# Performance work log

Hardware: AMD Instinct MI355X
Metric: run time of the kernel (lower is better)

## Reference

```python
import jax, jax.numpy as jnp
import numpy as np

B, V = 128, 128000

def setup_inputs() -> dict:
    key = jax.random.key(0)
    k1, k2, k3, k4 = jax.random.split(key, 4)
    logits = jax.random.normal(k1, (B, V), dtype=jnp.float32) * 4.0
    k = jax.random.randint(k2, (B,), 1, 64).astype(jnp.int32)
    p = jax.random.uniform(k3, (B,), dtype=jnp.float32, minval=0.5, maxval=1.0)
    # torch's q.exponential_(): Exp(1) noise = -log(U)
    u = jax.random.uniform(k4, (B, V), dtype=jnp.float32, minval=1e-10, maxval=1.0)
    exp_noise = -jnp.log(u)
    return {"logits": logits, "k": k, "p": p, "exp_noise": exp_noise}

def _apply_top_k_top_p(logits, k, p):
    # ascending sort, matching torch logits.sort(descending=False)
    idx = jnp.argsort(logits, axis=-1)                       # [B, V]
    logits_sort = jnp.take_along_axis(logits, idx, axis=-1)  # [B, V]
    # top-k: threshold is the (V-k)-th smallest value; everything below -> -inf
    thr_pos = (logits.shape[-1] - k.astype(jnp.int32))[:, None]       # [B, 1]
    thr = jnp.take_along_axis(logits_sort, thr_pos, axis=-1)          # [B, 1]
    logits_sort = jnp.where(logits_sort < thr, -jnp.inf, logits_sort)
    # top-p: drop the low-probability tail whose cumulative mass <= 1 - p
    probs_sort = jax.nn.softmax(logits_sort, axis=-1)
    probs_sum = jnp.cumsum(probs_sort, axis=-1)
    top_p_mask = probs_sum <= (1.0 - p)[:, None]
    top_p_mask = top_p_mask.at[:, -1].set(False)  # always keep the max token
    logits_sort = jnp.where(top_p_mask, -jnp.inf, logits_sort)
    # scatter filtered values back to original token positions
    inv = jnp.argsort(idx, axis=-1)
    return jnp.take_along_axis(logits_sort, inv, axis=-1)

def reference(logits, k, p, exp_noise):
    filtered = _apply_top_k_top_p(logits, k, p)
    probs = jax.nn.softmax(filtered.astype(jnp.float32), axis=-1)
    # random_sample: argmax(probs / Exp(1)) == Gumbel-trick categorical sample
    return jnp.argmax(probs / exp_noise, axis=-1)
```

## Files before the change

kernel.cpp:

```cpp
#include <hip/hip_runtime.h>
#include <stdint.h>

#define B_ROWS 128
#define V_COLS 128000
#define BPR 16
#define SLICE (V_COLS / BPR)
#define N4 (SLICE / 4)
#define K1_THREADS 256
#define CAP 2048

__device__ __forceinline__ uint32_t f2u_bits(uint32_t x) {
    return (x & 0x80000000u) ? ~x : (x | 0x80000000u);
}
__device__ __forceinline__ float u2f(uint32_t u) {
    uint32_t x = (u & 0x80000000u) ? (u & 0x7FFFFFFFu) : ~u;
    return __uint_as_float(x);
}

__device__ __forceinline__ bool pair_gt(uint32_t au, uint32_t ai, uint32_t bu, uint32_t bi) {
    return (au > bu) || (au == bu && ai > bi);
}

__device__ __forceinline__ void bitonic_sort_desc(uint32_t* su, uint32_t* si, int NP) {
    const int tid = threadIdx.x;
    const int nth = blockDim.x;
    for (int ksz = 2; ksz <= NP; ksz <<= 1) {
        for (int j = ksz >> 1; j > 0; j >>= 1) {
            __syncthreads();
            for (int i = tid; i < NP; i += nth) {
                int ixj = i ^ j;
                if (ixj > i) {
                    uint32_t ua = su[i], ub = su[ixj];
                    uint32_t ia = si[i], ib = si[ixj];
                    bool a_lt = (ua < ub) || (ua == ub && ia < ib);
                    if (((i & ksz) == 0) ? a_lt : !a_lt) {
                        su[i] = ub; su[ixj] = ua;
                        si[i] = ib; si[ixj] = ia;
                    }
                }
            }
        }
    }
    __syncthreads();
}

__device__ __forceinline__ void wave_sort64_pair_desc(uint32_t& u, uint32_t& i, int lane) {
    #pragma unroll
    for (int ksz = 2; ksz <= 64; ksz <<= 1) {
        #pragma unroll
        for (int j = ksz >> 1; j > 0; j >>= 1) {
            uint32_t ou = (uint32_t)__shfl_xor((int)u, j, 64);
            uint32_t oi = (uint32_t)__shfl_xor((int)i, j, 64);
            bool asc   = (lane & ksz) == 0;
            bool lower = (lane & j) == 0;
            bool self_gt = pair_gt(u, i, ou, oi);
            bool keep_self = (asc == lower) ? self_gt : !self_gt;
            if (!keep_self) { u = ou; i = oi; }
        }
    }
}

__device__ __forceinline__ void merge64_desc(uint32_t& au, uint32_t& ai,
                                             uint32_t bu, uint32_t bi, int lane) {
    uint32_t ou = (uint32_t)__shfl_xor((int)bu, 63, 64);
    uint32_t oi = (uint32_t)__shfl_xor((int)bi, 63, 64);
    if (!pair_gt(au, ai, ou, oi)) { au = ou; ai = oi; }
    #pragma unroll
    for (int j = 32; j >= 1; j >>= 1) {
        uint32_t cu = (uint32_t)__shfl_xor((int)au, j, 64);
        uint32_t ci = (uint32_t)__shfl_xor((int)ai, j, 64);
        bool self_gt = pair_gt(au, ai, cu, ci);
        bool keep_self = ((lane & j) == 0) ? self_gt : !self_gt;
        if (!keep_self) { au = cu; ai = ci; }
    }
}

__global__ __launch_bounds__(K1_THREADS) void topk_slice_kernel(
    const float* __restrict__ logits,
    uint32_t* __restrict__ out_u, uint32_t* __restrict__ out_idx)
{
    __shared__ uint32_t s_u[CAP];
    __shared__ uint32_t s_i[CAP];
    __shared__ uint32_t s_T[4];
    __shared__ int s_cnt;

    const int blk = blockIdx.x;
    const int row = blk >> 4;
    const int q   = blk & 15;
    const int tid = threadIdx.x;
    const int lane = tid & 63;
    const int wv   = tid >> 6;

    if (tid == 0) s_cnt = 0;

    const uint4* src = (const uint4*)(logits + (size_t)row * V_COLS + (size_t)q * SLICE);

    uint4 g[8];
    #pragma unroll
    for (int j = 0; j < 8; ++j) {
        int i4 = j * K1_THREADS + tid;
        i4 = (i4 < N4) ? i4 : (N4 - 1);
        g[j] = src[i4];
    }
    #pragma unroll
    for (int j = 0; j < 8; ++j) {
        g[j].x = f2u_bits(g[j].x); g[j].y = f2u_bits(g[j].y);
        g[j].z = f2u_bits(g[j].z); g[j].w = f2u_bits(g[j].w);
    }
    if (7 * K1_THREADS + tid >= N4) { g[7].x = 0u; g[7].y = 0u; g[7].z = 0u; g[7].w = 0u; }

    uint32_t mx = 0u;
    #pragma unroll
    for (int j = 0; j < 8; ++j) {
        uint32_t a = g[j].x > g[j].y ? g[j].x : g[j].y;
        uint32_t b = g[j].z > g[j].w ? g[j].z : g[j].w;
        a = a > b ? a : b;
        mx = mx > a ? mx : a;
    }

    uint32_t v = mx;
    #pragma unroll
    for (int ksz = 2; ksz <= 64; ksz <<= 1) {
        #pragma unroll
        for (int j = ksz >> 1; j > 0; j >>= 1) {
            uint32_t o = (uint32_t)__shfl_xor((int)v, j, 64);
            bool asc   = (lane & ksz) == 0;
            bool lower = (lane & j) == 0;
            uint32_t mn = (v < o) ? v : o;
            uint32_t mh = (v < o) ? o : v;
            v = (asc == lower) ? mn : mh;
        }
    }
    uint32_t Tw = (uint32_t)__shfl((int)v, 48, 64);
    if (lane == 0) s_T[wv] = Tw;
    __syncthreads();
    uint32_t T0 = s_T[0] < s_T[1] ? s_T[0] : s_T[1];
    uint32_t T1 = s_T[2] < s_T[3] ? s_T[2] : s_T[3];
    uint32_t T = T0 < T1 ? T0 : T1;

    #pragma unroll
    for (int j = 0; j < 8; ++j) {
        const int base = (j * K1_THREADS + tid) * 4;
        uint32_t uu0 = g[j].x, uu1 = g[j].y, uu2 = g[j].z, uu3 = g[j].w;
        if (uu0 >= T && uu0 != 0u) { int p = atomicAdd(&s_cnt, 1); if (p < CAP) { s_u[p] = uu0; s_i[p] = (uint32_t)(q * SLICE + base + 0); } }
        if (uu1 >= T && uu1 != 0u) { int p = atomicAdd(&s_cnt, 1); if (p < CAP) { s_u[p] = uu1; s_i[p] = (uint32_t)(q * SLICE + base + 1); } }
        if (uu2 >= T && uu2 != 0u) { int p = atomicAdd(&s_cnt, 1); if (p < CAP) { s_u[p] = uu2; s_i[p] = (uint32_t)(q * SLICE + base + 2); } }
        if (uu3 >= T && uu3 != 0u) { int p = atomicAdd(&s_cnt, 1); if (p < CAP) { s_u[p] = uu3; s_i[p] = (uint32_t)(q * SLICE + base + 3); } }
    }
    __syncthreads();
    int cnt = s_cnt; if (cnt > CAP) cnt = CAP;

    if (cnt <= 256) {
        for (int i = cnt + tid; i < 256; i += K1_THREADS) { s_u[i] = 0u; s_i[i] = 0xFFFFFFFFu; }
        __syncthreads();
        uint32_t cu = s_u[wv * 64 + lane];
        uint32_t ci = s_i[wv * 64 + lane];
        wave_sort64_pair_desc(cu, ci, lane);
        s_u[wv * 64 + lane] = cu;
        s_i[wv * 64 + lane] = ci;
        __syncthreads();
        if (wv == 0) {
            uint32_t b1u = s_u[64 + lane],  b1i = s_i[64 + lane];
            uint32_t b2u = s_u[128 + lane], b2i = s_i[128 + lane];
            uint32_t b3u = s_u[192 + lane], b3i = s_i[192 + lane];
            merge64_desc(cu, ci, b1u, b1i, lane);
            merge64_desc(b2u, b2i, b3u, b3i, lane);
            merge64_desc(cu, ci, b2u, b2i, lane);
            out_u[blk * 64 + lane]   = cu;
            out_idx[blk * 64 + lane] = ci;
        }
    } else {
        int NP = 256; while (NP < cnt) NP <<= 1;
        for (int i = cnt + tid; i < NP; i += K1_THREADS) { s_u[i] = 0u; s_i[i] = 0xFFFFFFFFu; }
        bitonic_sort_desc(s_u, s_i, NP);
        if (tid < 64) { out_u[blk * 64 + tid] = s_u[tid]; out_idx[blk * 64 + tid] = s_i[tid]; }
    }
}

__global__ __launch_bounds__(256) void sample_kernel(
    const uint32_t* __restrict__ in_u, const uint32_t* __restrict__ in_idx,
    const int* __restrict__ kk, const float* __restrict__ pp,
    const float* __restrict__ noise, int* __restrict__ out)
{
    __shared__ uint32_t m_u[4 * 64];
    __shared__ uint32_t m_i[4 * 64];
    const int row = blockIdx.x;
    const int tid = threadIdx.x;
    const int lane = tid & 63;
    const int wv   = tid >> 6;

    const uint32_t* bu = in_u  + (size_t)row * (BPR * 64);
    const uint32_t* bi = in_idx + (size_t)row * (BPR * 64);

    uint32_t a0u = bu[(wv * 4 + 0) * 64 + lane], a0i = bi[(wv * 4 + 0) * 64 + lane];
    uint32_t a1u = bu[(wv * 4 + 1) * 64 + lane], a1i = bi[(wv * 4 + 1) * 64 + lane];
    uint32_t a2u = bu[(wv * 4 + 2) * 64 + lane], a2i = bi[(wv * 4 + 2) * 64 + lane];
    uint32_t a3u = bu[(wv * 4 + 3) * 64 + lane], a3i = bi[(wv * 4 + 3) * 64 + lane];
    merge64_desc(a0u, a0i, a1u, a1i, lane);
    merge64_desc(a2u, a2i, a3u, a3i, lane);
    merge64_desc(a0u, a0i, a2u, a2i, lane);
    m_u[wv * 64 + lane] = a0u;
    m_i[wv * 64 + lane] = a0i;
    __syncthreads();

    if (wv == 0) {
        uint32_t b1u = m_u[64 + lane],  b1i = m_i[64 + lane];
        uint32_t b2u = m_u[128 + lane], b2i = m_i[128 + lane];
        uint32_t b3u = m_u[192 + lane], b3i = m_i[192 + lane];
        merge64_desc(a0u, a0i, b1u, b1i, lane);
        merge64_desc(b2u, b2i, b3u, b3i, lane);
        merge64_desc(a0u, a0i, b2u, b2i, lane);

        float v = u2f(a0u);
        uint32_t tok = a0i;
        int k = kk[row];
        if (k > 64) k = 64;
        float p = pp[row];

        float thrv = __shfl(v, k - 1, 64);
        bool kept = v >= thrv;
        float m = __shfl(v, 0, 64);
        float e = kept ? expf(v - m) : 0.0f;

        float denom = e;
        #pragma unroll
        for (int off = 1; off < 64; off <<= 1) denom += __shfl_xor(denom, off, 64);
        float prob = e / denom;

        float cums = prob;
        #pragma unroll
        for (int off = 1; off < 64; off <<= 1) {
            float o = __shfl_down(cums, off, 64);
            cums += (lane + off < 64) ? o : 0.0f;
        }
        bool masked = (cums <= 1.0f - p) && (lane != 0);
        bool surv = kept && !masked;

        float e2 = surv ? e : 0.0f;
        float denom2 = e2;
        #pragma unroll
        for (int off = 1; off < 64; off <<= 1) denom2 += __shfl_xor(denom2, off, 64);

        float score = -1.0f;
        uint32_t bidx = 0xFFFFFFFFu;
        if (surv) {
            float nz = noise[(size_t)row * V_COLS + tok];
            score = (e / denom2) / nz;
            bidx = tok;
        }
        #pragma unroll
        for (int off = 1; off < 64; off <<= 1) {
            float os = __shfl_xor(score, off, 64);
            uint32_t oi = __shfl_xor(bidx, off, 64);
            if (os > score || (os == score && oi < bidx)) { score = os; bidx = oi; }
        }
        if (lane == 0) out[row] = (int)bidx;
    }
}

extern "C" void kernel_launch(void* const* d_in, const int* in_sizes, int n_in,
                              void* d_out, int out_size, void* d_ws, size_t ws_size,
                              hipStream_t stream) {
    const float* logits = (const float*)d_in[0];
    const int* kk       = (const int*)d_in[1];
    const float* pp     = (const float*)d_in[2];
    const float* noise  = (const float*)d_in[3];
    int* out            = (int*)d_out;

    uint32_t* ws_u   = (uint32_t*)d_ws;
    uint32_t* ws_idx = ws_u + (size_t)B_ROWS * BPR * 64;

    topk_slice_kernel<<<B_ROWS * BPR, K1_THREADS, 0, stream>>>(logits, ws_u, ws_idx);
    sample_kernel<<<B_ROWS, 256, 0, stream>>>(ws_u, ws_idx, kk, pp, noise, out);
}
```

Baseline: 28.04 us.

## Fuse slice top-k and sampling kernels via last-block-per-row atomic counter

Merges the two launches into one kernel. Each slice block writes its top-64 candidates to workspace, then increments a per-row atomic counter, and the last block to arrive for a row does the merge and sampling. This removes the second kernel launch and the gap between kernels. The cost is threadfence and atomic traffic, plus reliance on the workspace counters starting at zero or at the 0xAAAAAAAA sentinel that the code handles. An empty asm barrier on the loaded registers is also added, presumably to force all global loads to be issued before any compute.

Result: slower. 73.85 us (+163.4%).

```diff
diff --git a/kernel.cpp b/kernel.cpp
--- a/kernel.cpp
+++ b/kernel.cpp
@@ -6,7 +6,7 @@
 #define BPR 16
 #define SLICE (V_COLS / BPR)
 #define N4 (SLICE / 4)
-#define K1_THREADS 256
+#define NTHR 256
 #define CAP 2048
 
 __device__ __forceinline__ uint32_t f2u_bits(uint32_t x) {
@@ -21,13 +21,43 @@
     return (au > bu) || (au == bu && ai > bi);
 }
 
-__device__ __forceinline__ void bitonic_sort_desc(uint32_t* su, uint32_t* si, int NP) {
+__device__ __forceinline__ void merge64(uint32_t& au, uint32_t& ai,
+                                        uint32_t bu, uint32_t bi, int lane) {
+    uint32_t ou = (uint32_t)__shfl_xor((int)bu, 63, 64);
+    uint32_t oi = (uint32_t)__shfl_xor((int)bi, 63, 64);
+    if (!pair_gt(au, ai, ou, oi)) { au = ou; ai = oi; }
+    #pragma unroll
+    for (int j = 32; j >= 1; j >>= 1) {
+        uint32_t cu = (uint32_t)__shfl_xor((int)au, j, 64);
+        uint32_t ci = (uint32_t)__shfl_xor((int)ai, j, 64);
+        bool sg = pair_gt(au, ai, cu, ci);
+        bool keep = ((lane & j) == 0) ? sg : !sg;
+        if (!keep) { au = cu; ai = ci; }
+    }
+}
+
+__device__ __forceinline__ void wave_sort64(uint32_t& u, uint32_t& i, int lane) {
+    #pragma unroll
+    for (int ksz = 2; ksz <= 64; ksz <<= 1) {
+        #pragma unroll
+        for (int j = ksz >> 1; j > 0; j >>= 1) {
+            uint32_t ou = (uint32_t)__shfl_xor((int)u, j, 64);
+            uint32_t oi = (uint32_t)__shfl_xor((int)i, j, 64);
+            bool asc   = (lane & ksz) == 0;
+            bool lower = (lane & j) == 0;
+            bool sg = pair_gt(u, i, ou, oi);
+            bool keep = (asc == lower) ? sg : !sg;
+            if (!keep) { u = ou; i = oi; }
+        }
+    }
+}
+
+__device__ __forceinline__ void lds_bitonic_desc(uint32_t* su, uint32_t* si, int NP) {
     const int tid = threadIdx.x;
-    const int nth = blockDim.x;
     for (int ksz = 2; ksz <= NP; ksz <<= 1) {
         for (int j = ksz >> 1; j > 0; j >>= 1) {
             __syncthreads();
-            for (int i = tid; i < NP; i += nth) {
+            for (int i = tid; i < NP; i += NTHR) {
                 int ixj = i ^ j;
                 if (ixj > i) {
                     uint32_t ua = su[i], ub = su[ixj];
@@ -44,45 +74,17 @@
     __syncthreads();
 }
 
-__device__ __forceinline__ void wave_sort64_pair_desc(uint32_t& u, uint32_t& i, int lane) {
-    #pragma unroll
-    for (int ksz = 2; ksz <= 64; ksz <<= 1) {
-        #pragma unroll
-        for (int j = ksz >> 1; j > 0; j >>= 1) {
-            uint32_t ou = (uint32_t)__shfl_xor((int)u, j, 64);
-            uint32_t oi = (uint32_t)__shfl_xor((int)i, j, 64);
-            bool asc   = (lane & ksz) == 0;
-            bool lower = (lane & j) == 0;
-            bool self_gt = pair_gt(u, i, ou, oi);
-            bool keep_self = (asc == lower) ? self_gt : !self_gt;
-            if (!keep_self) { u = ou; i = oi; }
-        }
-    }
-}
-
-__device__ __forceinline__ void merge64_desc(uint32_t& au, uint32_t& ai,
-                                             uint32_t bu, uint32_t bi, int lane) {
-    uint32_t ou = (uint32_t)__shfl_xor((int)bu, 63, 64);
-    uint32_t oi = (uint32_t)__shfl_xor((int)bi, 63, 64);
-    if (!pair_gt(au, ai, ou, oi)) { au = ou; ai = oi; }
-    #pragma unroll
-    for (int j = 32; j >= 1; j >>= 1) {
-        uint32_t cu = (uint32_t)__shfl_xor((int)au, j, 64);
-        uint32_t ci = (uint32_t)__shfl_xor((int)ai, j, 64);
-        bool self_gt = pair_gt(au, ai, cu, ci);
-        bool keep_self = ((lane & j) == 0) ? self_gt : !self_gt;
-        if (!keep_self) { au = cu; ai = ci; }
-    }
-}
-
-__global__ __launch_bounds__(K1_THREADS) void topk_slice_kernel(
-    const float* __restrict__ logits,
-    uint32_t* __restrict__ out_u, uint32_t* __restrict__ out_idx)
+__global__ __launch_bounds__(NTHR) void fused_topk_sample_kernel(
+    const float* __restrict__ logits, const int* __restrict__ kk,
+    const float* __restrict__ pp, const float* __restrict__ noise,
+    uint32_t* __restrict__ ws_u, uint32_t* __restrict__ ws_i,
+    unsigned int* __restrict__ counters, int* __restrict__ out)
 {
     __shared__ uint32_t s_u[CAP];
     __shared__ uint32_t s_i[CAP];
     __shared__ uint32_t s_T[4];
     __shared__ int s_cnt;
+    __shared__ int s_last;
 
     const int blk = blockIdx.x;
     const int row = blk >> 4;
@@ -98,16 +100,20 @@
     uint4 g[8];
     #pragma unroll
     for (int j = 0; j < 8; ++j) {
-        int i4 = j * K1_THREADS + tid;
+        int i4 = j * NTHR + tid;
         i4 = (i4 < N4) ? i4 : (N4 - 1);
         g[j] = src[i4];
     }
     #pragma unroll
+    for (int j = 0; j < 8; ++j)
+        asm volatile("" : "+v"(g[j].x), "+v"(g[j].y), "+v"(g[j].z), "+v"(g[j].w));
+
+    #pragma unroll
     for (int j = 0; j < 8; ++j) {
         g[j].x = f2u_bits(g[j].x); g[j].y = f2u_bits(g[j].y);
         g[j].z = f2u_bits(g[j].z); g[j].w = f2u_bits(g[j].w);
     }
-    if (7 * K1_THREADS + tid >= N4) { g[7].x = 0u; g[7].y = 0u; g[7].z = 0u; g[7].w = 0u; }
+    if (7 * NTHR + tid >= N4) { g[7].x = 0u; g[7].y = 0u; g[7].z = 0u; g[7].w = 0u; }
 
     uint32_t mx = 0u;
     #pragma unroll
@@ -140,87 +146,88 @@
 
     #pragma unroll
     for (int j = 0; j < 8; ++j) {
-        const int base = (j * K1_THREADS + tid) * 4;
+        const int base = q * SLICE + (j * NTHR + tid) * 4;
         uint32_t uu0 = g[j].x, uu1 = g[j].y, uu2 = g[j].z, uu3 = g[j].w;
-        if (uu0 >= T && uu0 != 0u) { int p = atomicAdd(&s_cnt, 1); if (p < CAP) { s_u[p] = uu0; s_i[p] = (uint32_t)(q * SLICE + base + 0); } }
-        if (uu1 >= T && uu1 != 0u) { int p = atomicAdd(&s_cnt, 1); if (p < CAP) { s_u[p] = uu1; s_i[p] = (uint32_t)(q * SLICE + base + 1); } }
-        if (uu2 >= T && uu2 != 0u) { int p = atomicAdd(&s_cnt, 1); if (p < CAP) { s_u[p] = uu2; s_i[p] = (uint32_t)(q * SLICE + base + 2); } }
-        if (uu3 >= T && uu3 != 0u) { int p = atomicAdd(&s_cnt, 1); if (p < CAP) { s_u[p] = uu3; s_i[p] = (uint32_t)(q * SLICE + base + 3); } }
+        if (uu0 >= T && uu0 != 0u) { int p = atomicAdd(&s_cnt, 1); if (p < CAP) { s_u[p] = uu0; s_i[p] = (uint32_t)(base + 0); } }
+        if (uu1 >= T && uu1 != 0u) { int p = atomicAdd(&s_cnt, 1); if (p < CAP) { s_u[p] = uu1; s_i[p] = (uint32_t)(base + 1); } }
+        if (uu2 >= T && uu2 != 0u) { int p = atomicAdd(&s_cnt, 1); if (p < CAP) { s_u[p] = uu2; s_i[p] = (uint32_t)(base + 2); } }
+        if (uu3 >= T && uu3 != 0u) { int p = atomicAdd(&s_cnt, 1); if (p < CAP) { s_u[p] = uu3; s_i[p] = (uint32_t)(base + 3); } }
     }
     __syncthreads();
     int cnt = s_cnt; if (cnt > CAP) cnt = CAP;
 
     if (cnt <= 256) {
-        for (int i = cnt + tid; i < 256; i += K1_THREADS) { s_u[i] = 0u; s_i[i] = 0xFFFFFFFFu; }
+        for (int i = cnt + tid; i < 256; i += NTHR) { s_u[i] = 0u; s_i[i] = 0xFFFFFFFFu; }
         __syncthreads();
         uint32_t cu = s_u[wv * 64 + lane];
         uint32_t ci = s_i[wv * 64 + lane];
-        wave_sort64_pair_desc(cu, ci, lane);
+        wave_sort64(cu, ci, lane);
         s_u[wv * 64 + lane] = cu;
         s_i[wv * 64 + lane] = ci;
         __syncthreads();
         if (wv == 0) {
-            uint32_t b1u = s_u[64 + lane],  b1i = s_i[64 + lane];
-            uint32_t b2u = s_u[128 + lane], b2i = s_i[128 + lane];
-            uint32_t b3u = s_u[192 + lane], b3i = s_i[192 + lane];
-            merge64_desc(cu, ci, b1u, b1i, lane);
-            merge64_desc(b2u, b2i, b3u, b3i, lane);
-            merge64_desc(cu, ci, b2u, b2i, lane);
-            out_u[blk * 64 + lane]   = cu;
-            out_idx[blk * 64 + lane] = ci;
+            uint32_t b1u = s_u[64 + lane];  uint32_t b1i = s_i[64 + lane];
+            uint32_t b2u = s_u[128 + lane]; uint32_t b2i = s_i[128 + lane];
+            uint32_t b3u = s_u[192 + lane]; uint32_t b3i = s_i[192 + lane];
+            merge64(cu, ci, b1u, b1i, lane);
+            merge64(b2u, b2i, b3u, b3i, lane);
+            merge64(cu, ci, b2u, b2i, lane);
+            ws_u[blk * 64 + lane] = cu;
+            ws_i[blk * 64 + lane] = ci;
         }
     } else {
         int NP = 256; while (NP < cnt) NP <<= 1;
-        for (int i = cnt + tid; i < NP; i += K1_THREADS) { s_u[i] = 0u; s_i[i] = 0xFFFFFFFFu; }
-        bitonic_sort_desc(s_u, s_i, NP);
-        if (tid < 64) { out_u[blk * 64 + tid] = s_u[tid]; out_idx[blk * 64 + tid] = s_i[tid]; }
-    }
-}
-
-__global__ __launch_bounds__(256) void sample_kernel(
-    const uint32_t* __restrict__ in_u, const uint32_t* __restrict__ in_idx,
-    const int* __restrict__ kk, const float* __restrict__ pp,
-    const float* __restrict__ noise, int* __restrict__ out)
-{
-    __shared__ uint32_t m_u[4 * 64];
-    __shared__ uint32_t m_i[4 * 64];
-    const int row = blockIdx.x;
-    const int tid = threadIdx.x;
-    const int lane = tid & 63;
-    const int wv   = tid >> 6;
-
-    const uint32_t* bu = in_u  + (size_t)row * (BPR * 64);
-    const uint32_t* bi = in_idx + (size_t)row * (BPR * 64);
-
-    uint32_t a0u = bu[(wv * 4 + 0) * 64 + lane], a0i = bi[(wv * 4 + 0) * 64 + lane];
-    uint32_t a1u = bu[(wv * 4 + 1) * 64 + lane], a1i = bi[(wv * 4 + 1) * 64 + lane];
-    uint32_t a2u = bu[(wv * 4 + 2) * 64 + lane], a2i = bi[(wv * 4 + 2) * 64 + lane];
-    uint32_t a3u = bu[(wv * 4 + 3) * 64 + lane], a3i = bi[(wv * 4 + 3) * 64 + lane];
-    merge64_desc(a0u, a0i, a1u, a1i, lane);
-    merge64_desc(a2u, a2i, a3u, a3i, lane);
-    merge64_desc(a0u, a0i, a2u, a2i, lane);
-    m_u[wv * 64 + lane] = a0u;
-    m_i[wv * 64 + lane] = a0i;
+        for (int i = cnt + tid; i < NP; i += NTHR) { s_u[i] = 0u; s_i[i] = 0xFFFFFFFFu; }
+        lds_bitonic_desc(s_u, s_i, NP);
+        if (tid < 64) { ws_u[blk * 64 + tid] = s_u[tid]; ws_i[blk * 64 + tid] = s_i[tid]; }
+    }
+    __syncthreads();
+
+    if (tid == 0) {
+        __threadfence();
+        unsigned int raw = atomicAdd(&counters[row], 1u);
+        unsigned int eff = (raw >= 0xAAAAAAAAu) ? (raw - 0xAAAAAAAAu) : raw;
+        s_last = (eff == 15u) ? 1 : 0;
+        if (s_last) {
+            counters[row] = 0u;
+            __threadfence();
+        }
+    }
+    __syncthreads();
+    if (!s_last) return;
+
+    const uint32_t* bu = ws_u + (size_t)row * (BPR * 64);
+    const uint32_t* bi = ws_i + (size_t)row * (BPR * 64);
+
+    uint32_t a0u = bu[(wv * 4 + 0) * 64 + lane]; uint32_t a0i = bi[(wv * 4 + 0) * 64 + lane];
+    uint32_t a1u = bu[(wv * 4 + 1) * 64 + lane]; uint32_t a1i = bi[(wv * 4 + 1) * 64 + lane];
+    uint32_t a2u = bu[(wv * 4 + 2) * 64 + lane]; uint32_t a2i = bi[(wv * 4 + 2) * 64 + lane];
+    uint32_t a3u = bu[(wv * 4 + 3) * 64 + lane]; uint32_t a3i = bi[(wv * 4 + 3) * 64 + lane];
+    merge64(a0u, a0i, a1u, a1i, lane);
+    merge64(a2u, a2i, a3u, a3i, lane);
+    merge64(a0u, a0i, a2u, a2i, lane);
+    s_u[wv * 64 + lane] = a0u;
+    s_i[wv * 64 + lane] = a0i;
     __syncthreads();
 
     if (wv == 0) {
-        uint32_t b1u = m_u[64 + lane],  b1i = m_i[64 + lane];
-        uint32_t b2u = m_u[128 + lane], b2i = m_i[128 + lane];
-        uint32_t b3u = m_u[192 + lane], b3i = m_i[192 + lane];
-        merge64_desc(a0u, a0i, b1u, b1i, lane);
-        merge64_desc(b2u, b2i, b3u, b3i, lane);
-        merge64_desc(a0u, a0i, b2u, b2i, lane);
-
-        float v = u2f(a0u);
+        uint32_t b1u = s_u[64 + lane];  uint32_t b1i = s_i[64 + lane];
+        uint32_t b2u = s_u[128 + lane]; uint32_t b2i = s_i[128 + lane];
+        uint32_t b3u = s_u[192 + lane]; uint32_t b3i = s_i[192 + lane];
+        merge64(a0u, a0i, b1u, b1i, lane);
+        merge64(b2u, b2i, b3u, b3i, lane);
+        merge64(a0u, a0i, b2u, b2i, lane);
+
+        float v2 = u2f(a0u);
         uint32_t tok = a0i;
         int k = kk[row];
         if (k > 64) k = 64;
         float p = pp[row];
 
-        float thrv = __shfl(v, k - 1, 64);
-        bool kept = v >= thrv;
-        float m = __shfl(v, 0, 64);
-        float e = kept ? expf(v - m) : 0.0f;
+        float thrv = __shfl(v2, k - 1, 64);
+        bool kept = v2 >= thrv;
+        float m = __shfl(v2, 0, 64);
+        float e = kept ? expf(v2 - m) : 0.0f;
 
         float denom = e;
         #pragma unroll
@@ -267,9 +274,10 @@
     const float* noise  = (const float*)d_in[3];
     int* out            = (int*)d_out;
 
-    uint32_t* ws_u   = (uint32_t*)d_ws;
-    uint32_t* ws_idx = ws_u + (size_t)B_ROWS * BPR * 64;
-
-    topk_slice_kernel<<<B_ROWS * BPR, K1_THREADS, 0, stream>>>(logits, ws_u, ws_idx);
-    sample_kernel<<<B_ROWS, 256, 0, stream>>>(ws_u, ws_idx, kk, pp, noise, out);
-}
+    uint32_t*     ws_u = (uint32_t*)d_ws;
+    uint32_t*     ws_i = (uint32_t*)d_ws + (size_t)B_ROWS * BPR * 64;
+    unsigned int* cnt  = (unsigned int*)d_ws + 2 * (size_t)B_ROWS * BPR * 64;
+
+    fused_topk_sample_kernel<<<B_ROWS * BPR, NTHR, 0, stream>>>(
+        logits, kk, pp, noise, ws_u, ws_i, cnt, out);
+}
```
